# Kernel optimization log

Measured on AMD Instinct MI355X. Metric: run time of the kernel, lower is better.

The kernel has to match this reference:

```python
import jax, jax.numpy as jnp
import numpy as np

SEQ_LEN = 12
B = 1024
NG = 32            # scenes
G = B // NG        # pedestrians per scene
E = 64             # embedding_dim
H = 128            # h_dim
PP = 512           # mlp_pre_pool hidden
BOT = 1024         # bottleneck_dim
MLPD = 1024        # mlp_dim


def _w(key, fan_in, shape):
    return jax.random.normal(key, shape, jnp.float32) / np.sqrt(fan_in)


def setup_inputs():
    key = jax.random.key(0)
    ks = jax.random.split(key, 16)
    starts = jnp.arange(NG, dtype=jnp.int32) * G
    inp = {
        'last_pos': jax.random.normal(ks[0], (B, 2), jnp.float32),
        'last_pos_rel': jax.random.normal(ks[1], (B, 2), jnp.float32) * 0.1,
        'decoder_h': jax.random.normal(ks[2], (1, B, H), jnp.float32) * 0.1,
        'decoder_c': jax.random.normal(ks[3], (1, B, H), jnp.float32) * 0.1,
        'seq_start_end': jnp.stack([starts, starts + G], axis=1),
        'W_emb': _w(ks[4], 2, (2, E)), 'b_emb': jnp.zeros((E,), jnp.float32),
        'W_ih': _w(ks[5], E, (4 * H, E)), 'b_ih': jnp.zeros((4 * H,), jnp.float32),
        'W_hh': _w(ks[6], H, (4 * H, H)), 'b_hh': jnp.zeros((4 * H,), jnp.float32),
        'W_h2p': _w(ks[7], H, (H, 2)), 'b_h2p': jnp.zeros((2,), jnp.float32),
        'W_sp': _w(ks[8], 2, (2, E)), 'b_sp': jnp.zeros((E,), jnp.float32),
        'W_pp1': _w(ks[9], E + H, (E + H, PP)), 'b_pp1': jnp.zeros((PP,), jnp.float32),
        'W_pp2': _w(ks[10], PP, (PP, BOT)), 'b_pp2': jnp.zeros((BOT,), jnp.float32),
        'W_m1': _w(ks[11], H + BOT, (H + BOT, MLPD)), 'b_m1': jnp.zeros((MLPD,), jnp.float32),
        'W_m2': _w(ks[12], MLPD, (MLPD, H)), 'b_m2': jnp.zeros((H,), jnp.float32),
    }
    return inp


def _forward(last_pos, last_pos_rel, h0, c0,
             W_emb, b_emb, W_ih, b_ih, W_hh, b_hh, W_h2p, b_h2p,
             W_sp, b_sp, W_pp1, b_pp1, W_pp2, b_pp2, W_m1, b_m1, W_m2, b_m2):
    relu = jax.nn.relu

    def pool_net(h, pos):
        # PoolHiddenNet over NG contiguous equal-size groups of G peds.
        hg = h.reshape(NG, G, H)
        pg = pos.reshape(NG, G, 2)
        # rel[g, i, j] = pos_j - pos_i  (matches repeat/tile ordering in torch code)
        rel = pg[:, None, :, :] - pg[:, :, None, :]          # [NG,G,G,2]
        emb = rel @ W_sp + b_sp                               # [NG,G,G,E]
        hj = jnp.broadcast_to(hg[:, None, :, :], (NG, G, G, H))
        x = jnp.concatenate([emb, hj], axis=-1)               # [NG,G,G,E+H]
        x = relu(x @ W_pp1 + b_pp1)
        x = relu(x @ W_pp2 + b_pp2)                           # [NG,G,G,BOT]
        return jnp.max(x, axis=2).reshape(B, BOT)             # max over neighbors j

    def lstm_cell(x, h, c):
        gates = x @ W_ih.T + b_ih + h @ W_hh.T + b_hh
        i, f, g, o = jnp.split(gates, 4, axis=-1)
        c2 = jax.nn.sigmoid(f) * c + jax.nn.sigmoid(i) * jnp.tanh(g)
        h2 = jax.nn.sigmoid(o) * jnp.tanh(c2)
        return h2, c2

    dec_in0 = last_pos_rel @ W_emb + b_emb

    def step(carry, _):
        lp, din, h, c = carry
        h, c = lstm_cell(din, h, c)
        rel_pos = h @ W_h2p + b_h2p                           # [B,2]
        curr_pos = rel_pos + lp
        pool_h = pool_net(h, curr_pos)                        # [B,BOT]
        hcat = jnp.concatenate([h, pool_h], axis=1)
        h = relu(relu(hcat @ W_m1 + b_m1) @ W_m2 + b_m2)      # refreshed decoder_h
        din = rel_pos @ W_emb + b_emb
        return (curr_pos, din, h, c), rel_pos

    (_, _, h_fin, _), pred = jax.lax.scan(
        step, (last_pos, dec_in0, h0, c0), None, length=SEQ_LEN)
    return pred, h_fin[None]                                  # [T,B,2], [1,B,H]


def reference(last_pos, last_pos_rel, decoder_h, decoder_c, seq_start_end,
              W_emb, b_emb, W_ih, b_ih, W_hh, b_hh, W_h2p, b_h2p,
              W_sp, b_sp, W_pp1, b_pp1, W_pp2, b_pp2, W_m1, b_m1, W_m2, b_m2):
    del seq_start_end  # uniform contiguous groups encoded statically (NG, G)
    return _forward(last_pos, last_pos_rel, decoder_h[0], decoder_c[0],
                    W_emb, b_emb, W_ih, b_ih, W_hh, b_hh, W_h2p, b_h2p,
                    W_sp, b_sp, W_pp1, b_pp1, W_pp2, b_pp2, W_m1, b_m1, W_m2, b_m2)
```

## Files before the change

### kernel.cpp

```cpp
#include <hip/hip_runtime.h>
#include <math.h>

#define T_SEQ 12

typedef __bf16 bf16x8 __attribute__((ext_vector_type(8)));
typedef float f32x4 __attribute__((ext_vector_type(4)));
typedef unsigned short u16x8 __attribute__((ext_vector_type(8)));

static __device__ __forceinline__ unsigned short bf16bits(float x) {
  return __builtin_bit_cast(unsigned short, (__bf16)x);
}

enum : int {
  OFF_LP    = 0,
  OFF_DIN   = 2048,
  OFF_C     = 198656,
  OFF_HDEC  = 329728,
  OFF_WC    = 460800,
  OFF_BC    = 461824,
  OFF_PW    = 462336,
  OFF_AA    = 986624,
  OFF_WP2T  = 1510912,
  OFF_WM1T  = 1773056,
  OFF_HCATB = 2362880,
  OFF_WM2TB = 2952704,
  OFF_MIDB  = 3018240,
  OFF_WIHT  = 3542528,
  OFF_WHHT  = 3575296,
  OFF_WFRAG = 3640832
};

#define SWZP(byte, row) ((byte) ^ (((row) & 7) << 4))

__global__ __launch_bounds__(256) void k_setup(
    const float* __restrict__ last_pos, const float* __restrict__ lpr,
    const float* __restrict__ dh, const float* __restrict__ dc,
    const float* __restrict__ W_emb, const float* __restrict__ b_emb,
    float* __restrict__ lp, float* __restrict__ din,
    float* __restrict__ h_dec, float* __restrict__ c) {
  int idx = blockIdx.x * 256 + threadIdx.x;
  if (idx < 2048) lp[idx] = last_pos[idx];
  h_dec[idx] = dh[idx];
  c[idx] = dc[idx];
  if (idx < 65536) {
    int b = idx >> 6, e = idx & 63;
    din[idx] = lpr[b*2] * W_emb[e] + lpr[b*2+1] * W_emb[64+e] + b_emb[e];
  }
}

__global__ __launch_bounds__(256) void k_wc(
    const float* __restrict__ W_sp, const float* __restrict__ b_sp,
    const float* __restrict__ W_pp1, const float* __restrict__ b_pp1,
    float* __restrict__ Wc, float* __restrict__ bc) {
  int n = blockIdx.x * 256 + threadIdx.x;
  if (n >= 512) return;
  float a0 = 0.f, a1 = 0.f, ab = 0.f;
#pragma unroll 8
  for (int k = 0; k < 64; k++) {
    float w = W_pp1[k*512 + n];
    a0 += W_sp[k] * w;
    a1 += W_sp[64+k] * w;
    ab += b_sp[k] * w;
  }
  Wc[n] = a0; Wc[512+n] = a1; bc[n] = ab + b_pp1[n];
}

__global__ __launch_bounds__(256) void k_tcvt(
    const float* __restrict__ src, unsigned short* __restrict__ dst,
    int R, int C) {
  __shared__ float t[32][33];
  const int bx = blockIdx.x * 32, by = blockIdx.y * 32;
  const int tx = threadIdx.x & 31, ty = threadIdx.x >> 5;
#pragma unroll
  for (int i = 0; i < 32; i += 8) t[ty+i][tx] = src[(size_t)(by+ty+i)*C + bx+tx];
  __syncthreads();
#pragma unroll
  for (int i = 0; i < 32; i += 8)
    dst[(size_t)(bx+ty+i)*R + by+tx] = bf16bits(t[tx][ty+i]);
}

__global__ __launch_bounds__(256) void k_t32(
    const float* __restrict__ src, float* __restrict__ dst, int R, int C) {
  __shared__ float t[32][33];
  const int bx = blockIdx.x * 32, by = blockIdx.y * 32;
  const int tx = threadIdx.x & 31, ty = threadIdx.x >> 5;
#pragma unroll
  for (int i = 0; i < 32; i += 8) t[ty+i][tx] = src[(size_t)(by+ty+i)*C + bx+tx];
  __syncthreads();
#pragma unroll
  for (int i = 0; i < 32; i += 8)
    dst[(size_t)(bx+ty+i)*R + by+tx] = t[tx][ty+i];
}

__global__ __launch_bounds__(256) void k_frag(
    const unsigned short* __restrict__ Wp2t, unsigned short* __restrict__ Wfrag) {
  const int tid = blockIdx.x * 256 + threadIdx.x;
  const int fid = tid >> 6, l = tid & 63;
  const int nbb = fid >> 4, ks = fid & 15;
  u16x8 v = *(const u16x8*)(Wp2t + (size_t)(nbb*16 + (l & 15))*512 +
                            ks*32 + (l >> 4)*8);
  *(u16x8*)(Wfrag + (size_t)tid*8) = v;
}

__global__ __launch_bounds__(512) void k_step1(
    float* __restrict__ din, const float* __restrict__ h_dec,
    float* __restrict__ cst, unsigned short* __restrict__ hcatB,
    float* __restrict__ lp, float* __restrict__ pred,
    const float* __restrict__ Wiht, const float* __restrict__ b_ih,
    const float* __restrict__ Whht, const float* __restrict__ b_hh,
    const float* __restrict__ W_h2p, const float* __restrict__ b_h2p,
    const float* __restrict__ W_emb, const float* __restrict__ b_emb,
    const float* __restrict__ W1b, const float* __restrict__ Wc,
    const float* __restrict__ bc,
    float* __restrict__ PW, float* __restrict__ Aa, int t) {
  const int b0 = blockIdx.x * 4;
  const int tid = threadIdx.x;
  __shared__ float xh[4*192];
  __shared__ float gl[4*512];
  __shared__ float hbuf[4*128];
  __shared__ float relS[8], curS[8];

  for (int i = tid; i < 768; i += 512) {
    int r = i / 192, k = i - r*192;
    xh[i] = (k < 64) ? din[(b0+r)*64 + k] : h_dec[(b0+r)*128 + k - 64];
  }
  __syncthreads();
  {
    const int n = tid;
    float bias = b_ih[n] + b_hh[n];
    float acc[4] = {bias, bias, bias, bias};
#pragma unroll 8
    for (int k = 0; k < 64; k++) {
      float wv = Wiht[k*512 + n];
#pragma unroll
      for (int r = 0; r < 4; r++) acc[r] += xh[r*192 + k] * wv;
    }
#pragma unroll 8
    for (int k = 0; k < 128; k++) {
      float wv = Whht[k*512 + n];
#pragma unroll
      for (int r = 0; r < 4; r++) acc[r] += xh[r*192 + 64 + k] * wv;
    }
#pragma unroll
    for (int r = 0; r < 4; r++) gl[r*512 + n] = acc[r];
  }
  __syncthreads();
  {
    int r = tid >> 7, hh = tid & 127;
    float ig = gl[r*512 + hh],       fg = gl[r*512 + 128 + hh];
    float gg = gl[r*512 + 256 + hh], og = gl[r*512 + 384 + hh];
    ig = 1.f/(1.f+expf(-ig)); fg = 1.f/(1.f+expf(-fg));
    gg = tanhf(gg);           og = 1.f/(1.f+expf(-og));
    int row = b0 + r;
    float c2 = fg * cst[row*128 + hh] + ig * gg;
    float h2 = og * tanhf(c2);
    cst[row*128 + hh] = c2;
    hbuf[r*128 + hh] = h2;
    hcatB[(size_t)row*1152 + hh] = bf16bits(h2);
  }
  __syncthreads();
  if (tid < 128) {
    int r = tid >> 5, col = (tid >> 4) & 1, l16 = tid & 15;
    float s = 0.f;
    for (int k = l16; k < 128; k += 16) s += hbuf[r*128 + k] * W_h2p[k*2 + col];
#pragma unroll
    for (int off = 8; off > 0; off >>= 1) s += __shfl_xor(s, off);
    if (l16 == 0) {
      float rel = s + b_h2p[col];
      float old = lp[(b0+r)*2 + col];
      relS[r*2 + col] = rel;
      curS[r*2 + col] = old + rel;
      lp[(b0+r)*2 + col] = old + rel;
      pred[t*2048 + (b0+r)*2 + col] = rel;
    }
  }
  __syncthreads();
  if (tid < 256) {
    int r = tid >> 6, e = tid & 63;
    din[(b0+r)*64 + e] = relS[r*2]*W_emb[e] + relS[r*2+1]*W_emb[64+e] + b_emb[e];
  }
  {
    const int n = tid;
    float acc[4] = {0.f, 0.f, 0.f, 0.f};
#pragma unroll 4
    for (int k = 0; k < 128; k++) {
      float wv = W1b[k*512 + n];
#pragma unroll
      for (int r = 0; r < 4; r++) acc[r] += hbuf[r*128 + k] * wv;
    }
    float wc0 = Wc[n], wc1 = Wc[512+n], bcv = bc[n];
#pragma unroll
    for (int r = 0; r < 4; r++) {
      float pw = curS[r*2]*wc0 + curS[r*2+1]*wc1;
      PW[(size_t)(b0+r)*512 + n] = pw;
      Aa[(size_t)(b0+r)*512 + n] = acc[r] + pw + bcv;
    }
  }
}

__global__ __launch_bounds__(512) void k_pool8(
    const float* __restrict__ Aa, const float* __restrict__ PW,
    const unsigned short* __restrict__ Wfrag, const float* __restrict__ bp2,
    unsigned short* __restrict__ hcatB) {
  const int bid = blockIdx.x;
  const int mt = (bid >> 3) & 7;
  const int g  = (bid & 7) + ((bid >> 6) << 3);
  const int tid = threadIdx.x, lane = tid & 63, w = tid >> 6;
  const int wr = w >> 2, wc = w & 3;
  const int l15 = lane & 15, lhi = lane >> 4;
  __shared__ __align__(128) char lds[163840];
  char* As = lds;
  char* B0 = lds + 131072;
  char* B1 = lds + 131072 + 16384;

  {
    const int ke = lane * 8;
#pragma unroll 4
    for (int rr = 0; rr < 16; rr++) {
      const int r = rr * 8 + w;
      const int j = r & 31, ii = r >> 5;
      const float* aRow = Aa + (size_t)(g*32 + j)*512 + ke;
      const float* pRow = PW + (size_t)(g*32 + mt*4 + ii)*512 + ke;
      float4 a0 = *(const float4*)aRow;
      float4 a1 = *(const float4*)(aRow + 4);
      float4 p0 = *(const float4*)pRow;
      float4 p1 = *(const float4*)(pRow + 4);
      bf16x8 y;
      y[0] = (__bf16)fmaxf(a0.x - p0.x, 0.f);
      y[1] = (__bf16)fmaxf(a0.y - p0.y, 0.f);
      y[2] = (__bf16)fmaxf(a0.z - p0.z, 0.f);
      y[3] = (__bf16)fmaxf(a0.w - p0.w, 0.f);
      y[4] = (__bf16)fmaxf(a1.x - p1.x, 0.f);
      y[5] = (__bf16)fmaxf(a1.y - p1.y, 0.f);
      y[6] = (__bf16)fmaxf(a1.z - p1.z, 0.f);
      y[7] = (__bf16)fmaxf(a1.w - p1.w, 0.f);
      *(bf16x8*)(As + SWZP(r*1024 + lane*16, r)) = y;
    }
  }

  const int u0 = tid, u1 = tid + 512;
  const size_t gfo0 = (size_t)((u0 >> 6) * 16) * 512 + (u0 & 63) * 8;
  const size_t gfo1 = (size_t)((u1 >> 6) * 16) * 512 + (u1 & 63) * 8;

  {
    u16x8 s0 = *(const u16x8*)(Wfrag + gfo0);
    u16x8 s1 = *(const u16x8*)(Wfrag + gfo1);
    *(u16x8*)(B0 + u0*16) = s0;
    *(u16x8*)(B0 + u1*16) = s1;
  }
  u16x8 r0, r1;
  {
    const size_t base = (size_t)512;
    r0 = *(const u16x8*)(Wfrag + base + gfo0);
    r1 = *(const u16x8*)(Wfrag + base + gfo1);
  }
  __syncthreads();

  for (int nt = 0; nt < 4; nt++) {
    f32x4 acc[4][4] = {};
    for (int k0 = 0; k0 < 16; k0++) {
      const int q = nt*16 + k0;
      char* Bcur = (q & 1) ? B1 : B0;
      char* Bnxt = (q & 1) ? B0 : B1;
      if (q < 63) {
        *(u16x8*)(Bnxt + u0*16) = r0;
        *(u16x8*)(Bnxt + u1*16) = r1;
      }
      if (q < 62) {
        const int q2 = q + 2;
        const size_t base = (size_t)((q2 >> 4) * 256 + (q2 & 15)) * 512;
        r0 = *(const u16x8*)(Wfrag + base + gfo0);
        r1 = *(const u16x8*)(Wfrag + base + gfo1);
      }
      bf16x8 af[4], bfr[4];
#pragma unroll
      for (int mf = 0; mf < 4; mf++) {
        const int row = wr*64 + mf*16 + l15;
        af[mf] = *(const bf16x8*)(As + SWZP(row*1024 + k0*64 + lhi*16, row));
      }
#pragma unroll
      for (int nf = 0; nf < 4; nf++)
        bfr[nf] = *(const bf16x8*)(Bcur + (wc*4 + nf)*1024 + lane*16);
#pragma unroll
      for (int mf = 0; mf < 4; mf++)
#pragma unroll
        for (int nf = 0; nf < 4; nf++)
          acc[mf][nf] = __builtin_amdgcn_mfma_f32_16x16x32_bf16(
              af[mf], bfr[nf], acc[mf][nf], 0, 0, 0);
      __syncthreads();
    }
#pragma unroll
    for (int isub = 0; isub < 2; isub++)
#pragma unroll
      for (int nf = 0; nf < 4; nf++) {
        f32x4 v0 = acc[isub*2][nf], v1 = acc[isub*2 + 1][nf];
        float mx = fmaxf(fmaxf(fmaxf(v0[0], v0[1]), fmaxf(v0[2], v0[3])),
                         fmaxf(fmaxf(v1[0], v1[1]), fmaxf(v1[2], v1[3])));
        mx = fmaxf(mx, __shfl_xor(mx, 16));
        mx = fmaxf(mx, __shfl_xor(mx, 32));
        if (lane < 16) {
          const int n = nt*256 + wc*64 + nf*16 + lane;
          const int i = mt*4 + wr*2 + isub;
          hcatB[(size_t)(g*32 + i)*1152 + 128 + n] =
              bf16bits(fmaxf(mx + bp2[n], 0.f));
        }
      }
  }
}

__global__ __launch_bounds__(256) void k_m1k(
    const unsigned short* __restrict__ A, const unsigned short* __restrict__ Bw,
    const float* __restrict__ bias, unsigned short* __restrict__ outB) {
  const int nt = blockIdx.x, mt = blockIdx.y;
  const int tid = threadIdx.x, lane = tid & 63, w = tid >> 6;
  const int l15 = lane & 15, lhi = lane >> 4;
  __shared__ __align__(128) char lds[65536];
  const unsigned short* aSrc = A  + (size_t)(mt*64)*1152;
  const unsigned short* bSrc = Bw + (size_t)(nt*64)*1152;

  u16x8 rg[8];
#pragma unroll
  for (int p = 0; p < 8; p++) {
    const int u = tid + p*256;
    const int isB = u >> 10, v = u & 1023;
    const int row = v >> 4, slot = v & 15;
    u16x8 val = *(const u16x8*)((isB ? bSrc : aSrc) + (size_t)row*1152 + slot*8);
    *(u16x8*)(lds + isB*16384 + SWZP(row*256 + slot*16, row)) = val;
  }
#pragma unroll
  for (int p = 0; p < 8; p++) {
    const int u = tid + p*256;
    const int isB = u >> 10, v = u & 1023;
    const int row = v >> 4, slot = v & 15;
    rg[p] = *(const u16x8*)((isB ? bSrc : aSrc) + (size_t)row*1152 + 128 + slot*8);
  }
  __syncthreads();

  f32x4 acc[4][4] = {};
  for (int c = 0; c < 9; c++) {
    const int cur = (c & 1) * 32768;
    const int nxt = 32768 - cur;
    if (c < 8) {
#pragma unroll
      for (int p = 0; p < 8; p++) {
        const int u = tid + p*256;
        const int isB = u >> 10, v = u & 1023;
        const int row = v >> 4, slot = v & 15;
        *(u16x8*)(lds + nxt + isB*16384 + SWZP(row*256 + slot*16, row)) = rg[p];
      }
    }
    if (c < 7) {
#pragma unroll
      for (int p = 0; p < 8; p++) {
        const int u = tid + p*256;
        const int isB = u >> 10, v = u & 1023;
        const int row = v >> 4, slot = v & 15;
        rg[p] = *(const u16x8*)((isB ? bSrc : aSrc) + (size_t)row*1152 +
                                (c+2)*128 + slot*8);
      }
    }
    bf16x8 af[4], bf[4];
#pragma unroll
    for (int mf = 0; mf < 4; mf++) {
      const int row = mf*16 + l15;
      af[mf] = *(const bf16x8*)(lds + cur + SWZP(row*256 + w*64 + lhi*16, row));
    }
#pragma unroll
    for (int nf = 0; nf < 4; nf++) {
      const int row = nf*16 + l15;
      bf[nf] = *(const bf16x8*)(lds + cur + 16384 +
                                SWZP(row*256 + w*64 + lhi*16, row));
    }
#pragma unroll
    for (int mf = 0; mf < 4; mf++)
#pragma unroll
      for (int nf = 0; nf < 4; nf++)
        acc[mf][nf] = __builtin_amdgcn_mfma_f32_16x16x32_bf16(
            af[mf], bf[nf], acc[mf][nf], 0, 0, 0);
    __syncthreads();
  }

#pragma unroll
  for (int mf = 0; mf < 4; mf++)
#pragma unroll
    for (int nf = 0; nf < 4; nf++)
      *(f32x4*)(lds + w*16384 + (mf*4 + nf)*1024 + lane*16) = acc[mf][nf];
  __syncthreads();
#pragma unroll
  for (int pi = 0; pi < 4; pi++) {
    const int p = w*4 + pi;
    f32x4 s = *(const f32x4*)(lds + p*1024 + lane*16);
#pragma unroll
    for (int wv = 1; wv < 4; wv++) {
      f32x4 q = *(const f32x4*)(lds + wv*16384 + p*1024 + lane*16);
      s[0] += q[0]; s[1] += q[1]; s[2] += q[2]; s[3] += q[3];
    }
    const int col = nt*64 + (p & 3)*16 + l15;
    const float bv = bias[col];
#pragma unroll
    for (int r = 0; r < 4; r++) {
      const int row = mt*64 + (p >> 2)*16 + lhi*4 + r;
      outB[(size_t)row*1024 + col] = bf16bits(fmaxf(s[r] + bv, 0.f));
    }
  }
}

__global__ __launch_bounds__(256) void k_m2k(
    const unsigned short* __restrict__ A, const unsigned short* __restrict__ Bw,
    const float* __restrict__ bias, float* __restrict__ hd,
    float* __restrict__ out, int last) {
  const int nt = blockIdx.x, mt = blockIdx.y;
  const int tid = threadIdx.x, lane = tid & 63, w = tid >> 6;
  const int l15 = lane & 15, lhi = lane >> 4;
  __shared__ __align__(128) char lds[49152];
  const unsigned short* aSrc = A  + (size_t)(mt*32)*1024;
  const unsigned short* bSrc = Bw + (size_t)(nt*64)*1024;

  u16x8 rg[6];
#pragma unroll
  for (int p = 0; p < 6; p++) {
    const int u = tid + p*256;
    const int isB = (u >= 512);
    const int v = isB ? (u - 512) : u;
    const int row = v >> 4, slot = v & 15;
    u16x8 val = *(const u16x8*)((isB ? bSrc : aSrc) + (size_t)row*1024 + slot*8);
    *(u16x8*)(lds + isB*8192 + SWZP(row*256 + slot*16, row)) = val;
  }
#pragma unroll
  for (int p = 0; p < 6; p++) {
    const int u = tid + p*256;
    const int isB = (u >= 512);
    const int v = isB ? (u - 512) : u;
    const int row = v >> 4, slot = v & 15;
    rg[p] = *(const u16x8*)((isB ? bSrc : aSrc) + (size_t)row*1024 + 128 + slot*8);
  }
  __syncthreads();

  f32x4 acc[2][4] = {};
  for (int c = 0; c < 8; c++) {
    const int cur = (c & 1) * 24576;
    const int nxt = 24576 - cur;
    if (c < 7) {
#pragma unroll
      for (int p = 0; p < 6; p++) {
        const int u = tid + p*256;
        const int isB = (u >= 512);
        const int v = isB ? (u - 512) : u;
        const int row = v >> 4, slot = v & 15;
        *(u16x8*)(lds + nxt + isB*8192 + SWZP(row*256 + slot*16, row)) = rg[p];
      }
    }
    if (c < 6) {
#pragma unroll
      for (int p = 0; p < 6; p++) {
        const int u = tid + p*256;
        const int isB = (u >= 512);
        const int v = isB ? (u - 512) : u;
        const int row = v >> 4, slot = v & 15;
        rg[p] = *(const u16x8*)((isB ? bSrc : aSrc) + (size_t)row*1024 +
                                (c+2)*128 + slot*8);
      }
    }
    bf16x8 af[2], bf[4];
#pragma unroll
    for (int mf = 0; mf < 2; mf++) {
      const int row = mf*16 + l15;
      af[mf] = *(const bf16x8*)(lds + cur + SWZP(row*256 + w*64 + lhi*16, row));
    }
#pragma unroll
    for (int nf = 0; nf < 4; nf++) {
      const int row = nf*16 + l15;
      bf[nf] = *(const bf16x8*)(lds + cur + 8192 +
                                SWZP(row*256 + w*64 + lhi*16, row));
    }
#pragma unroll
    for (int mf = 0; mf < 2; mf++)
#pragma unroll
      for (int nf = 0; nf < 4; nf++)
        acc[mf][nf] = __builtin_amdgcn_mfma_f32_16x16x32_bf16(
            af[mf], bf[nf], acc[mf][nf], 0, 0, 0);
    __syncthreads();
  }

#pragma unroll
  for (int mf = 0; mf < 2; mf++)
#pragma unroll
    for (int nf = 0; nf < 4; nf++)
      *(f32x4*)(lds + w*8192 + (mf*4 + nf)*1024 + lane*16) = acc[mf][nf];
  __syncthreads();
#pragma unroll
  for (int pi = 0; pi < 2; pi++) {
    const int p = w*2 + pi;
    f32x4 s = *(const f32x4*)(lds + p*1024 + lane*16);
#pragma unroll
    for (int wv = 1; wv < 4; wv++) {
      f32x4 q = *(const f32x4*)(lds + wv*8192 + p*1024 + lane*16);
      s[0] += q[0]; s[1] += q[1]; s[2] += q[2]; s[3] += q[3];
    }
    const int col = nt*64 + (p & 3)*16 + l15;
    const float bv = bias[col];
#pragma unroll
    for (int r = 0; r < 4; r++) {
      const int row = mt*32 + (p >> 2)*16 + lhi*4 + r;
      float v = fmaxf(s[r] + bv, 0.f);
      hd[(size_t)row*128 + col] = v;
      if (last) out[24576 + (size_t)row*128 + col] = v;
    }
  }
}

extern "C" void kernel_launch(void* const* d_in, const int* in_sizes, int n_in,
                              void* d_out, int out_size, void* d_ws, size_t ws_size,
                              hipStream_t stream) {
  const float* last_pos = (const float*)d_in[0];
  const float* lpr      = (const float*)d_in[1];
  const float* dh       = (const float*)d_in[2];
  const float* dc       = (const float*)d_in[3];
  const float* W_emb = (const float*)d_in[5];
  const float* b_emb = (const float*)d_in[6];
  const float* W_ih  = (const float*)d_in[7];
  const float* b_ih  = (const float*)d_in[8];
  const float* W_hh  = (const float*)d_in[9];
  const float* b_hh  = (const float*)d_in[10];
  const float* W_h2p = (const float*)d_in[11];
  const float* b_h2p = (const float*)d_in[12];
  const float* W_sp  = (const float*)d_in[13];
  const float* b_sp  = (const float*)d_in[14];
  const float* W_pp1 = (const float*)d_in[15];
  const float* b_pp1 = (const float*)d_in[16];
  const float* W_pp2 = (const float*)d_in[17];
  const float* b_pp2 = (const float*)d_in[18];
  const float* W_m1  = (const float*)d_in[19];
  const float* b_m1  = (const float*)d_in[20];
  const float* W_m2  = (const float*)d_in[21];
  const float* b_m2  = (const float*)d_in[22];

  float* ws    = (float*)d_ws;
  float* lp    = ws + OFF_LP;
  float* din   = ws + OFF_DIN;
  float* cst   = ws + OFF_C;
  float* h_dec = ws + OFF_HDEC;
  float* Wc    = ws + OFF_WC;
  float* bc    = ws + OFF_BC;
  float* PW    = ws + OFF_PW;
  float* Aa    = ws + OFF_AA;
  unsigned short* Wp2t  = (unsigned short*)(ws + OFF_WP2T);
  unsigned short* Wm1t  = (unsigned short*)(ws + OFF_WM1T);
  unsigned short* hcatB = (unsigned short*)(ws + OFF_HCATB);
  unsigned short* Wm2tB = (unsigned short*)(ws + OFF_WM2TB);
  unsigned short* midB  = (unsigned short*)(ws + OFF_MIDB);
  float* Wiht  = ws + OFF_WIHT;
  float* Whht  = ws + OFF_WHHT;
  unsigned short* Wfrag = (unsigned short*)(ws + OFF_WFRAG);
  float* out   = (float*)d_out;

  k_setup<<<512, 256, 0, stream>>>(last_pos, lpr, dh, dc, W_emb, b_emb, lp, din, h_dec, cst);
  k_wc<<<2, 256, 0, stream>>>(W_sp, b_sp, W_pp1, b_pp1, Wc, bc);
  { dim3 gt(32, 16); k_tcvt<<<gt, 256, 0, stream>>>(W_pp2, Wp2t, 512, 1024); }
  { dim3 gt(32, 36); k_tcvt<<<gt, 256, 0, stream>>>(W_m1, Wm1t, 1152, 1024); }
  { dim3 gt(4, 32);  k_tcvt<<<gt, 256, 0, stream>>>(W_m2, Wm2tB, 1024, 128); }
  { dim3 gt(2, 16);  k_t32<<<gt, 256, 0, stream>>>(W_ih, Wiht, 512, 64); }
  { dim3 gt(4, 16);  k_t32<<<gt, 256, 0, stream>>>(W_hh, Whht, 512, 128); }
  k_frag<<<256, 256, 0, stream>>>(Wp2t, Wfrag);

  for (int t = 0; t < T_SEQ; t++) {
    k_step1<<<256, 512, 0, stream>>>(din, h_dec, cst, hcatB, lp, out,
                                     Wiht, b_ih, Whht, b_hh, W_h2p, b_h2p,
                                     W_emb, b_emb, W_pp1 + 64*512, Wc, bc,
                                     PW, Aa, t);
    k_pool8<<<256, 512, 0, stream>>>(Aa, PW, Wfrag, b_pp2, hcatB);
    { dim3 gm(16, 16); k_m1k<<<gm, 256, 0, stream>>>(hcatB, Wm1t, b_m1, midB); }
    { dim3 gm(2, 32);  k_m2k<<<gm, 256, 0, stream>>>(midB, Wm2tB, b_m2, h_dec,
                                                     out, t == T_SEQ-1); }
  }
}
```

Measured before the change: 964.4 us.

## Load pool B fragments directly into registers with 4-deep prefetch, drop LDS staging

The pooling MFMA kernel no longer stages W_pp2 fragments through double-buffered shared memory with a block barrier every k-step. Each wave now loads its own B fragments straight from global memory into a 4-slot register ring, prefetching four steps ahead. This removes 16 __syncthreads per n-tile, shrinks LDS from 160KB to 128KB, and fully unrolls the k loop. In exchange, each wave issues redundant global/L2 reads (the four row-waves sharing a column fetch the same data), and register pressure rises by 16 vector registers per thread.

```diff
diff --git a/kernel.cpp b/kernel.cpp
--- a/kernel.cpp
+++ b/kernel.cpp
@@ -9,6 +9,9 @@
 
 static __device__ __forceinline__ unsigned short bf16bits(float x) {
   return __builtin_bit_cast(unsigned short, (__bf16)x);
+}
+static __device__ __forceinline__ bf16x8 asbf(u16x8 v) {
+  return __builtin_bit_cast(bf16x8, v);
 }
 
 enum : int {
@@ -198,7 +201,7 @@
   }
 }
 
-__global__ __launch_bounds__(512) void k_pool8(
+__global__ __launch_bounds__(512) void k_pool10(
     const float* __restrict__ Aa, const float* __restrict__ PW,
     const unsigned short* __restrict__ Wfrag, const float* __restrict__ bp2,
     unsigned short* __restrict__ hcatB) {
@@ -208,10 +211,7 @@
   const int tid = threadIdx.x, lane = tid & 63, w = tid >> 6;
   const int wr = w >> 2, wc = w & 3;
   const int l15 = lane & 15, lhi = lane >> 4;
-  __shared__ __align__(128) char lds[163840];
-  char* As = lds;
-  char* B0 = lds + 131072;
-  char* B1 = lds + 131072 + 16384;
+  __shared__ __align__(128) char As[131072];
 
   {
     const int ke = lane * 8;
@@ -237,57 +237,45 @@
       *(bf16x8*)(As + SWZP(r*1024 + lane*16, r)) = y;
     }
   }
-
-  const int u0 = tid, u1 = tid + 512;
-  const size_t gfo0 = (size_t)((u0 >> 6) * 16) * 512 + (u0 & 63) * 8;
-  const size_t gfo1 = (size_t)((u1 >> 6) * 16) * 512 + (u1 & 63) * 8;
-
-  {
-    u16x8 s0 = *(const u16x8*)(Wfrag + gfo0);
-    u16x8 s1 = *(const u16x8*)(Wfrag + gfo1);
-    *(u16x8*)(B0 + u0*16) = s0;
-    *(u16x8*)(B0 + u1*16) = s1;
-  }
-  u16x8 r0, r1;
-  {
-    const size_t base = (size_t)512;
-    r0 = *(const u16x8*)(Wfrag + base + gfo0);
-    r1 = *(const u16x8*)(Wfrag + base + gfo1);
-  }
-  __syncthreads();
+  __syncthreads();
+
+  const int nbase = wc * 4;
+  u16x8 bq[4][4];
+#pragma unroll
+  for (int d = 0; d < 4; d++)
+#pragma unroll
+    for (int nf = 0; nf < 4; nf++)
+      bq[d][nf] = *(const u16x8*)(Wfrag +
+          ((size_t)((nbase + nf)*16 + d))*512 + lane*8);
 
   for (int nt = 0; nt < 4; nt++) {
     f32x4 acc[4][4] = {};
+#pragma unroll
     for (int k0 = 0; k0 < 16; k0++) {
-      const int q = nt*16 + k0;
-      char* Bcur = (q & 1) ? B1 : B0;
-      char* Bnxt = (q & 1) ? B0 : B1;
-      if (q < 63) {
-        *(u16x8*)(Bnxt + u0*16) = r0;
-        *(u16x8*)(Bnxt + u1*16) = r1;
-      }
-      if (q < 62) {
-        const int q2 = q + 2;
-        const size_t base = (size_t)((q2 >> 4) * 256 + (q2 & 15)) * 512;
-        r0 = *(const u16x8*)(Wfrag + base + gfo0);
-        r1 = *(const u16x8*)(Wfrag + base + gfo1);
-      }
-      bf16x8 af[4], bfr[4];
+      const int slot = k0 & 3;
+      bf16x8 bfr[4];
+#pragma unroll
+      for (int nf = 0; nf < 4; nf++) bfr[nf] = asbf(bq[slot][nf]);
+      bf16x8 af[4];
 #pragma unroll
       for (int mf = 0; mf < 4; mf++) {
         const int row = wr*64 + mf*16 + l15;
         af[mf] = *(const bf16x8*)(As + SWZP(row*1024 + k0*64 + lhi*16, row));
       }
-#pragma unroll
-      for (int nf = 0; nf < 4; nf++)
-        bfr[nf] = *(const bf16x8*)(Bcur + (wc*4 + nf)*1024 + lane*16);
+      const int q4 = nt*16 + k0 + 4;
+      if (q4 < 64) {
+        const int nt4 = q4 >> 4, k4 = q4 & 15;
+#pragma unroll
+        for (int nf = 0; nf < 4; nf++)
+          bq[slot][nf] = *(const u16x8*)(Wfrag +
+              ((size_t)((nt4*16 + nbase + nf)*16 + k4))*512 + lane*8);
+      }
 #pragma unroll
       for (int mf = 0; mf < 4; mf++)
 #pragma unroll
         for (int nf = 0; nf < 4; nf++)
           acc[mf][nf] = __builtin_amdgcn_mfma_f32_16x16x32_bf16(
               af[mf], bfr[nf], acc[mf][nf], 0, 0, 0);
-      __syncthreads();
     }
 #pragma unroll
     for (int isub = 0; isub < 2; isub++)
@@ -568,7 +556,7 @@
                                      Wiht, b_ih, Whht, b_hh, W_h2p, b_h2p,
                                      W_emb, b_emb, W_pp1 + 64*512, Wc, bc,
                                      PW, Aa, t);
-    k_pool8<<<256, 512, 0, stream>>>(Aa, PW, Wfrag, b_pp2, hcatB);
+    k_pool10<<<256, 512, 0, stream>>>(Aa, PW, Wfrag, b_pp2, hcatB);
     { dim3 gm(16, 16); k_m1k<<<gm, 256, 0, stream>>>(hcatB, Wm1t, b_m1, midB); }
     { dim3 gm(2, 32);  k_m2k<<<gm, 256, 0, stream>>>(midB, Wm2tB, b_m2, h_dec,
                                                      out, t == T_SEQ-1); }
```

After: 1.588 ms. +64.7%, slower.
